# Kernel optimization log

Hardware: AMD Instinct MI355X
Metric: run time of the kernel (lower is better)

## Reference

```python
import jax, jax.numpy as jnp
import numpy as np

EPS = 1e-8

def setup_inputs() -> dict:
    key = jax.random.key(0)
    k1, k2 = jax.random.split(key)
    x1 = jax.random.normal(k1, (16, 4096, 256), dtype=jnp.float32)
    x2 = jax.random.normal(k2, (16, 4096, 256), dtype=jnp.float32)
    return {"x1": x1, "x2": x2}

def _l2_normalize(x):
    # matches F.normalize / torch norm-with-clamp: x / max(||x||, eps)
    n = jnp.linalg.norm(x, axis=-1, keepdims=True)
    return x / jnp.maximum(n, EPS)

def reference(x1, x2):
    # cosine distance: mean over all segment pairs of (1 - cos_sim)
    # mean_{i,j} (1 - x1n_i . x2n_j) == 1 - (mean_i x1n_i) . (mean_j x2n_j)
    # -- algebraically identical to the original per-batch mm + mean,
    # but avoids materializing the O(n_seg^2) similarity matrix.
    n_batch, embedding_dim = x1.shape[0], x1.shape[-1]
    x1 = x1.reshape(n_batch, -1, embedding_dim)
    x2 = x2.reshape(n_batch, -1, embedding_dim)
    x1n = _l2_normalize(x1)  # (B, S, D)
    x2n = _l2_normalize(x2)
    m1 = x1n.mean(axis=1)    # (B, D)
    m2 = x2n.mean(axis=1)    # (B, D)
    return 1.0 - jnp.einsum('bd,bd->b', m1, m2)  # (B,)
```

## Files before the change

### kernel.cpp

```cpp
#include <hip/hip_runtime.h>


constexpr int D = 256;
constexpr int S = 4096;
constexpr int B = 16;
constexpr int BLOCKS_PER_PAIR = 32;
constexpr int WAVES_PER_BLOCK = 4;
constexpr int WAVES_PER_PAIR  = BLOCKS_PER_PAIR * WAVES_PER_BLOCK;
constexpr int ROWS_PER_WAVE   = S / WAVES_PER_PAIR;
constexpr float EPS = 1e-8f;

__global__ __launch_bounds__(256) void row_norm_sum_kernel(
    const float* __restrict__ x1, const float* __restrict__ x2,
    float* __restrict__ sums )
{
    const int pair = blockIdx.x / BLOCKS_PER_PAIR;
    const int blk  = blockIdx.x % BLOCKS_PER_PAIR;
    const int w    = threadIdx.x >> 6;
    const int lane = threadIdx.x & 63;
    const int wv   = blk * WAVES_PER_BLOCK + w;

    const int batch = pair >> 1;
    const float* __restrict__ src = (pair & 1) ? x2 : x1;
    src += (size_t)batch * S * D;

    float4 acc = make_float4(0.f, 0.f, 0.f, 0.f);

    #pragma unroll
    for (int i = 0; i < ROWS_PER_WAVE; i += 2) {
        const int r0 = wv + (i + 0) * WAVES_PER_PAIR;
        const int r1 = wv + (i + 1) * WAVES_PER_PAIR;
        const float4 v0 = *(const float4*)(src + (size_t)r0 * D + lane * 4);
        const float4 v1 = *(const float4*)(src + (size_t)r1 * D + lane * 4);

        float ss0 = v0.x * v0.x + v0.y * v0.y + v0.z * v0.z + v0.w * v0.w;
        float ss1 = v1.x * v1.x + v1.y * v1.y + v1.z * v1.z + v1.w * v1.w;
        #pragma unroll
        for (int m = 1; m < 64; m <<= 1) {
            ss0 += __shfl_xor(ss0, m, 64);
            ss1 += __shfl_xor(ss1, m, 64);
        }
        const float s0 = 1.0f / fmaxf(sqrtf(ss0), EPS);
        const float s1 = 1.0f / fmaxf(sqrtf(ss1), EPS);
        acc.x += v0.x * s0 + v1.x * s1;
        acc.y += v0.y * s0 + v1.y * s1;
        acc.z += v0.z * s0 + v1.z * s1;
        acc.w += v0.w * s0 + v1.w * s1;
    }

    __shared__ float lds[WAVES_PER_BLOCK][D];
    *(float4*)&lds[w][lane * 4] = acc;
    __syncthreads();

    const int t = threadIdx.x;
    const float v = lds[0][t] + lds[1][t] + lds[2][t] + lds[3][t];
    atomicAdd(&sums[(size_t)pair * D + t], v);
}

__global__ __launch_bounds__(64) void finalize_kernel(
    const float* __restrict__ sums, float* __restrict__ out)
{
    const int b = blockIdx.x;
    const int lane = threadIdx.x;
    const float4 a = *(const float4*)(sums + (size_t)(2 * b + 0) * D + lane * 4);
    const float4 c = *(const float4*)(sums + (size_t)(2 * b + 1) * D + lane * 4);
    float d = a.x * c.x + a.y * c.y + a.z * c.z + a.w * c.w;
    #pragma unroll
    for (int m = 1; m < 64; m <<= 1) d += __shfl_xor(d, m, 64);
    if (lane == 0) {
        const float inv = 1.0f / ((float)S * (float)S);
        out[b] = 1.0f - d * inv;
    }
}

extern "C" void kernel_launch(void* const* d_in, const int* in_sizes, int n_in,
                              void* d_out, int out_size, void* d_ws, size_t ws_size,
                              hipStream_t stream) {
    const float* x1 = (const float*)d_in[0];
    const float* x2 = (const float*)d_in[1];
    float* out = (float*)d_out;
    float* sums = (float*)d_ws;

    hipMemsetAsync(sums, 0, (size_t)2 * B * D * sizeof(float), stream);

    row_norm_sum_kernel<<<2 * B * BLOCKS_PER_PAIR, 256, 0, stream>>>(x1, x2, sums);
    finalize_kernel<<<B, 64, 0, stream>>>(sums, out);
}
```

Before: 155.1 us.

## Write per-block partials instead of atomics, drop memset, double blocks, batch 4 rows

The row-normalize-sum kernel now writes per-block partial sums to workspace, and a new finalize kernel reduces them, which removes the memset and the global atomics when the workspace is large enough. It also doubles blocks per pair, processes four rows per iteration to put more loads in flight, and replaces sqrt-plus-divide with rsqrt on a squared epsilon. The kernel is memory-bound on about 134 MB of reads, so the gains come mainly from fewer launches and better latency hiding. The cost is a larger workspace and a slightly heavier finalize pass.

```diff
diff --git a/kernel.cpp b/kernel.cpp
--- a/kernel.cpp
+++ b/kernel.cpp
@@ -4,12 +4,15 @@
 constexpr int D = 256;
 constexpr int S = 4096;
 constexpr int B = 16;
-constexpr int BLOCKS_PER_PAIR = 32;
+constexpr int BLOCKS_PER_PAIR = 64;
 constexpr int WAVES_PER_BLOCK = 4;
 constexpr int WAVES_PER_PAIR  = BLOCKS_PER_PAIR * WAVES_PER_BLOCK;
 constexpr int ROWS_PER_WAVE   = S / WAVES_PER_PAIR;
-constexpr float EPS = 1e-8f;
+constexpr int NPAIR = 2 * B;
+constexpr int NBLK1 = NPAIR * BLOCKS_PER_PAIR;
+constexpr float EPS2 = 1e-16f;
 
+template <bool USE_PARTIALS>
 __global__ __launch_bounds__(256) void row_norm_sum_kernel(
     const float* __restrict__ x1, const float* __restrict__ x2,
     float* __restrict__ sums )
@@ -27,25 +30,32 @@
     float4 acc = make_float4(0.f, 0.f, 0.f, 0.f);
 
     #pragma unroll
-    for (int i = 0; i < ROWS_PER_WAVE; i += 2) {
-        const int r0 = wv + (i + 0) * WAVES_PER_PAIR;
-        const int r1 = wv + (i + 1) * WAVES_PER_PAIR;
-        const float4 v0 = *(const float4*)(src + (size_t)r0 * D + lane * 4);
-        const float4 v1 = *(const float4*)(src + (size_t)r1 * D + lane * 4);
-
-        float ss0 = v0.x * v0.x + v0.y * v0.y + v0.z * v0.z + v0.w * v0.w;
-        float ss1 = v1.x * v1.x + v1.y * v1.y + v1.z * v1.z + v1.w * v1.w;
+    for (int i = 0; i < ROWS_PER_WAVE; i += 4) {
+        float4 v[4];
+        float  ss[4];
+        #pragma unroll
+        for (int k = 0; k < 4; ++k) {
+            const int r = wv + (i + k) * WAVES_PER_PAIR;
+            v[k] = *(const float4*)(src + (size_t)r * D + lane * 4);
+        }
+        #pragma unroll
+        for (int k = 0; k < 4; ++k)
+            ss[k] = v[k].x * v[k].x + v[k].y * v[k].y
+                  + v[k].z * v[k].z + v[k].w * v[k].w;
         #pragma unroll
         for (int m = 1; m < 64; m <<= 1) {
-            ss0 += __shfl_xor(ss0, m, 64);
-            ss1 += __shfl_xor(ss1, m, 64);
+            #pragma unroll
+            for (int k = 0; k < 4; ++k)
+                ss[k] += __shfl_xor(ss[k], m, 64);
         }
-        const float s0 = 1.0f / fmaxf(sqrtf(ss0), EPS);
-        const float s1 = 1.0f / fmaxf(sqrtf(ss1), EPS);
-        acc.x += v0.x * s0 + v1.x * s1;
-        acc.y += v0.y * s0 + v1.y * s1;
-        acc.z += v0.z * s0 + v1.z * s1;
-        acc.w += v0.w * s0 + v1.w * s1;
+        #pragma unroll
+        for (int k = 0; k < 4; ++k) {
+            const float s = rsqrtf(fmaxf(ss[k], EPS2));
+            acc.x += v[k].x * s;
+            acc.y += v[k].y * s;
+            acc.z += v[k].z * s;
+            acc.w += v[k].w * s;
+        }
     }
 
     __shared__ float lds[WAVES_PER_BLOCK][D];
@@ -53,8 +63,40 @@
     __syncthreads();
 
     const int t = threadIdx.x;
-    const float v = lds[0][t] + lds[1][t] + lds[2][t] + lds[3][t];
-    atomicAdd(&sums[(size_t)pair * D + t], v);
+    const float val = lds[0][t] + lds[1][t] + lds[2][t] + lds[3][t];
+    if (USE_PARTIALS) {
+        sums[(size_t)blockIdx.x * D + t] = val;
+    } else {
+        atomicAdd(&sums[(size_t)pair * D + t], val);
+    }
+}
+
+__global__ __launch_bounds__(256) void finalize_partials_kernel(
+    const float* __restrict__ partials, float* __restrict__ out)
+{
+    const int b = blockIdx.x;
+    const int t = threadIdx.x;
+    const int w = t >> 6, lane = t & 63;
+
+    const float* p1 = partials + ((size_t)(2 * b + 0) * BLOCKS_PER_PAIR) * D + t;
+    const float* p2 = partials + ((size_t)(2 * b + 1) * BLOCKS_PER_PAIR) * D + t;
+    float s1 = 0.f, s2 = 0.f;
+    #pragma unroll 8
+    for (int k = 0; k < BLOCKS_PER_PAIR; ++k) {
+        s1 += p1[(size_t)k * D];
+        s2 += p2[(size_t)k * D];
+    }
+    float d = s1 * s2;
+    #pragma unroll
+    for (int m = 1; m < 64; m <<= 1) d += __shfl_xor(d, m, 64);
+
+    __shared__ float r[WAVES_PER_BLOCK];
+    if (lane == 0) r[w] = d;
+    __syncthreads();
+    if (t == 0) {
+        const float inv = 1.0f / ((float)S * (float)S);
+        out[b] = 1.0f - (r[0] + r[1] + r[2] + r[3]) * inv;
+    }
 }
 
 __global__ __launch_bounds__(64) void finalize_kernel(
@@ -79,10 +121,15 @@
     const float* x1 = (const float*)d_in[0];
     const float* x2 = (const float*)d_in[1];
     float* out = (float*)d_out;
-    float* sums = (float*)d_ws;
+    float* ws = (float*)d_ws;
 
-    hipMemsetAsync(sums, 0, (size_t)2 * B * D * sizeof(float), stream);
-
-    row_norm_sum_kernel<<<2 * B * BLOCKS_PER_PAIR, 256, 0, stream>>>(x1, x2, sums);
-    finalize_kernel<<<B, 64, 0, stream>>>(sums, out);
+    const size_t partial_bytes = (size_t)NBLK1 * D * sizeof(float);
+    if (ws_size >= partial_bytes) {
+        row_norm_sum_kernel<true><<<NBLK1, 256, 0, stream>>>(x1, x2, ws);
+        finalize_partials_kernel<<<B, 256, 0, stream>>>(ws, out);
+    } else {
+        hipMemsetAsync(ws, 0, (size_t)NPAIR * D * sizeof(float), stream);
+        row_norm_sum_kernel<false><<<NBLK1, 256, 0, stream>>>(x1, x2, ws);
+        finalize_kernel<<<B, 64, 0, stream>>>(ws, out);
+    }
 }
```

Measured after the change: 146.7 us, median of 2. 5.4% less time.
